# Performance work log

Hardware: AMD Instinct MI355X
Metric: run time of the kernel (lower is better)

Reference implementation:

```python
import jax, jax.numpy as jnp
import numpy as np

B, S, T1, V = 32, 60, 60, 50000   # batch, post len, response len (decoder runs T1-1 steps), vocab
E, A, H, ATT, DI = 300, 300, 512, 512, 512  # word emb, affect emb, rnn hidden, attention size, decoder input


def setup_inputs() -> dict:
    key = jax.random.key(0)
    ks = jax.random.split(key, 20)
    p = lambda i, shape: jax.random.normal(ks[i], shape, jnp.float32) * 0.02
    z = lambda n: jnp.zeros((n,), jnp.float32)
    return {
        'posts': jax.random.randint(ks[0], (B, S), 0, V),
        'responses': jax.random.randint(ks[1], (B, T1), 0, V),
        'len_posts': jnp.full((B,), S, jnp.int32),
        'emb': p(2, (V, E)), 'affect_emb': p(3, (V, A)),
        'enc_Wi': p(4, (3 * H, E)), 'enc_Wh': p(5, (3 * H, H)), 'enc_bi': z(3 * H), 'enc_bh': z(3 * H),
        'aff_Wi': p(6, (3 * H, A)), 'aff_Wh': p(7, (3 * H, H)), 'aff_bi': z(3 * H), 'aff_bh': z(3 * H),
        'Wp': p(8, (H, 2 * H)), 'bp': z(H),
        'Wl': p(9, (DI, E + H + ATT)), 'bl': z(DI),
        'dec_Wi': p(10, (3 * H, DI)), 'dec_Wh': p(11, (3 * H, H)), 'dec_bi': z(3 * H), 'dec_bh': z(3 * H),
        'Wa': p(12, (H, H)), 'Wc': p(13, (ATT, H)), 'bc': z(ATT),
        'Wv': p(14, (V, H + ATT)), 'bv': z(V),
    }


def _gru_cell(x, h, Wi, Wh, bi, bh):
    gi = x @ Wi.T + bi
    gh = h @ Wh.T + bh
    ir, iz, inn = jnp.split(gi, 3, -1)
    hr, hz, hn = jnp.split(gh, 3, -1)
    r = jax.nn.sigmoid(ir + hr)
    zg = jax.nn.sigmoid(iz + hz)
    n = jnp.tanh(inn + r * hn)
    return (1.0 - zg) * n + zg * h


def _gru_seq(xs, h0, Wi, Wh, bi, bh):
    # xs: [S, B, in] -> (outputs [S,B,H], h_last [B,H])
    def step(h, x):
        h2 = _gru_cell(x, h, Wi, Wh, bi, bh)
        return h2, h2
    hT, ys = jax.lax.scan(step, h0, xs)
    return ys, hT


def reference(posts, responses, len_posts, emb, affect_emb,
              enc_Wi, enc_Wh, enc_bi, enc_bh,
              aff_Wi, aff_Wh, aff_bi, aff_bh,
              Wp, bp, Wl, bl,
              dec_Wi, dec_Wh, dec_bi, dec_bh,
              Wa, Wc, bc, Wv, bv):
    embed_posts = emb[posts]            # [B,S,E]
    affect_posts = affect_emb[posts]    # [B,S,A]
    h0 = jnp.zeros((posts.shape[0], H), embed_posts.dtype)

    _, state_encoder = _gru_seq(embed_posts.transpose(1, 0, 2), h0, enc_Wi, enc_Wh, enc_bi, enc_bh)
    out_affect, state_affect = _gru_seq(affect_posts.transpose(1, 0, 2), h0, aff_Wi, aff_Wh, aff_bi, aff_bh)
    context_affect = out_affect[-1]     # [B,H] (all lengths == S)
    K = out_affect.transpose(1, 0, 2)   # [B,S,H] attention keys/values

    # PrepareState: Linear + tanh on concat of both encoder final states
    state0 = jnp.tanh(jnp.concatenate([state_encoder, state_affect], -1) @ Wp.T + bp)

    dec_in = emb[responses[:, :-1]].transpose(1, 0, 2)  # [T,B,E]
    init_attn = jnp.zeros((posts.shape[0], ATT), embed_posts.dtype)

    def dec_step(carry, x_emb):
        h, attn = carry
        x = jnp.concatenate([x_emb, context_affect, attn], -1) @ Wl.T + bl
        h = _gru_cell(x, h, dec_Wi, dec_Wh, dec_bi, dec_bh)
        scores = jnp.einsum('bd,bsd->bs', h @ Wa, K)        # Luong 'general'
        w = jax.nn.softmax(scores, -1)
        ctx = jnp.einsum('bs,bsd->bd', w, K)
        attn = jnp.tanh(ctx @ Wc.T + bc)
        return (h, attn), (jnp.concatenate([h, attn], -1), w)

    _, (outs, weights) = jax.lax.scan(dec_step, (state0, init_attn), dec_in)
    outs = outs.transpose(1, 0, 2)          # [B,T,H+ATT]
    weights = weights.transpose(1, 0, 2)    # [B,T,S]
    output_vocab = jax.nn.softmax(outs @ Wv.T + bv, -1)  # [B,T,V]
    return output_vocab, weights
```

## Files before the change

kernel.cpp:

```cpp
#include <hip/hip_runtime.h>

typedef unsigned int uint32;
typedef unsigned short u16;
typedef unsigned long long u64;
typedef __attribute__((ext_vector_type(8))) short bf8;
typedef __attribute__((ext_vector_type(4))) float f4;
typedef __attribute__((ext_vector_type(4))) uint32 u32x4;

#define DEV static __device__ __forceinline__

DEV f4 MFMA(bf8 a, bf8 b, f4 c) {
  return __builtin_amdgcn_mfma_f32_16x16x32_bf16(a, b, c, 0, 0, 0);
}
DEV u16 f2bf(float f) {
  uint32 u = __float_as_uint(f);
  return (u16)((u + 0x7FFFu + ((u >> 16) & 1u)) >> 16);
}
DEV float bf2f(u16 h) { return __uint_as_float(((uint32)h) << 16); }
DEV float bfLO(uint32 u) { return __uint_as_float(u << 16); }
DEV float bfHI(uint32 u) { return __uint_as_float(u & 0xFFFF0000u); }
DEV float sigmoid_(float x) { return 1.f / (1.f + __expf(-x)); }
DEV float tanh_(float x) {
  float cx = fminf(fmaxf(x, -15.f), 15.f);
  float e = __expf(2.f * cx);
  return (e - 1.f) / (e + 1.f);
}

DEV u64 ldA64(const void* p) {
  return __hip_atomic_load((u64*)p, __ATOMIC_RELAXED, __HIP_MEMORY_SCOPE_AGENT);
}
DEV void stA64(void* p, u64 v) {
  __hip_atomic_store((u64*)p, v, __ATOMIC_RELAXED, __HIP_MEMORY_SCOPE_AGENT);
}
DEV bf8 pk_frag(u64 lo, u64 hi) {
  u32x4 v = {(uint32)lo, (uint32)(lo >> 32), (uint32)hi, (uint32)(hi >> 32)};
  return __builtin_bit_cast(bf8, v);
}

DEV void wait_vm0() { asm volatile("s_waitcnt vmcnt(0)" ::: "memory"); }
DEV void arrive_rlx(int* f) {
  __hip_atomic_fetch_add(f, 1, __ATOMIC_RELAXED, __HIP_MEMORY_SCOPE_AGENT);
}
DEV void wait_rlx(int* f, int tgt) {
  for (int i = 0; i < (1 << 20); ++i) {
    if (__hip_atomic_load(f, __ATOMIC_RELAXED, __HIP_MEMORY_SCOPE_AGENT) >= tgt) return;
    __builtin_amdgcn_s_sleep(1);
  }
}

namespace L {
constexpr size_t o_flags  = 0;
constexpr size_t o_rowsum = 4096;
constexpr size_t o_bcomb  = 11776;
constexpr size_t o_gistat = 17920;
constexpr size_t o_xbuf   = 214528;
constexpr size_t o_henc   = 345600;
constexpr size_t o_haff   = 411136;
constexpr size_t o_cat    = 476672;
constexpr size_t o_Kbuf   = 542208;
constexpr size_t o_KA     = 2508288;
constexpr size_t o_embP   = 4474368;
constexpr size_t o_embA   = 5703168;
constexpr size_t o_embD   = 6931968;
constexpr size_t o_encWi  = 8140288;
constexpr size_t o_affWi  = 9123328;
constexpr size_t o_Whe    = 10106368;
constexpr size_t o_Wha    = 11679232;
constexpr size_t o_decWi  = 13252096;
constexpr size_t o_WlT    = 14824960;
constexpr size_t o_Wa     = 16184832;
constexpr size_t o_Wp     = 16709120;
constexpr size_t o_wq     = 17757696;
constexpr size_t o_Wcomb  = 18281984;
constexpr size_t o_WdE    = 26441216;
constexpr size_t o_WdA    = 27424256;
constexpr size_t o_Wd2    = 28997120;
constexpr size_t o_giE    = 32142848;
constexpr size_t o_giA    = 43939328;
constexpr size_t o_giD    = 55735808;
constexpr size_t o_outsB  = 67335680;
constexpr size_t o_WvB    = 71267840;
constexpr size_t WS_FULL  = 174028288;
constexpr size_t WOFF = 94400000;
}

__global__ __launch_bounds__(256) void kp_gather(
    const int* __restrict__ posts, const int* __restrict__ resp,
    const float* __restrict__ emb, const float* __restrict__ aemb, char* ws)
{
  using namespace L;
  const int gid = blockIdx.x * 256 + threadIdx.x;
  const int r = gid / 320, e = gid - r * 320;
  u16* embP = (u16*)(ws + o_embP);
  u16* embA = (u16*)(ws + o_embA);
  u16* embD = (u16*)(ws + o_embD);
  if (r < 1920) {
    const int b = r & 31, s = r >> 5;
    const int tok = posts[b * 60 + s];
    embP[r * 320 + e] = f2bf(e < 300 ? emb[(size_t)tok * 300 + e] : 0.f);
    embA[r * 320 + e] = f2bf(e < 300 ? aemb[(size_t)tok * 300 + e] : 0.f);
  } else if (r < 3808) {
    const int r2 = r - 1920;
    const int b = r2 & 31, t = r2 >> 5;
    const int tok = resp[b * 60 + t];
    embD[r2 * 320 + e] = f2bf(e < 300 ? emb[(size_t)tok * 300 + e] : 0.f);
  }
}

__global__ __launch_bounds__(256) void kp_wconv(
    const float* __restrict__ encWi, const float* __restrict__ affWi,
    const float* __restrict__ encWh, const float* __restrict__ affWh,
    const float* __restrict__ dWi, const float* __restrict__ Wl,
    const float* __restrict__ Wa, const float* __restrict__ Wp,
    const float* __restrict__ Wc, char* ws)
{
  using namespace L;
  long gid = (long)blockIdx.x * 256 + threadIdx.x;
  if (gid < 983040) {
    const int g = gid >= 491520;
    const long u = gid - (g ? 491520 : 0);
    const int n = (int)(u / 320), e = (int)(u - (long)n * 320);
    const float* src = g ? affWi : encWi;
    u16* dst = (u16*)(ws + (g ? o_affWi : o_encWi));
    dst[u] = f2bf(e < 300 ? src[(size_t)n * 300 + e] : 0.f);
    return;
  }
  gid -= 983040;
  if (gid < 2359296) {
    const int g = (int)(gid / 786432);
    const long u = gid - (long)g * 786432;
    const float* src = g == 0 ? encWh : (g == 1 ? affWh : dWi);
    u16* dst = (u16*)(ws + (g == 0 ? o_Whe : (g == 1 ? o_Wha : o_decWi)));
    dst[u] = f2bf(src[u]);
    return;
  }
  gid -= 2359296;
  if (gid < 679936) {
    const int j = (int)(gid >> 9), k = (int)(gid & 511);
    ((u16*)(ws + o_WlT))[gid] = f2bf(j < 1324 ? Wl[(size_t)k * 1324 + j] : 0.f);
    return;
  }
  gid -= 679936;
  if (gid < 262144) { ((u16*)(ws + o_Wa))[gid] = f2bf(Wa[gid]); return; }
  gid -= 262144;
  if (gid < 524288) { ((u16*)(ws + o_Wp))[gid] = f2bf(Wp[gid]); return; }
  gid -= 524288;
  if (gid < 131072) {
    const int q = (int)(gid & 3), j = (int)((gid >> 2) & 511), g4 = (int)(gid >> 11);
    const int d0 = g4 * 8 + q * 2;
    const uint32 lo = f2bf(Wc[(size_t)j * 512 + d0]);
    const uint32 hi = f2bf(Wc[(size_t)j * 512 + d0 + 1]);
    ((uint32*)(ws + o_wq))[gid] = lo | (hi << 16);
    return;
  }
  gid -= 131072;
  if (gid < 2944) {
    if (gid < 1024) ((uint32*)(ws + o_flags))[gid] = 0;
    else ((uint32*)(ws + o_rowsum))[gid - 1024] = 0;
    return;
  }
  gid -= 2944;
  if (gid < 49152) {
    if (gid < 16384) ((uint32*)(ws + o_outsB + (size_t)1888 * 1024 * 2))[gid] = 0;
    else if (gid < 32768) ((uint32*)(ws + o_henc))[gid - 16384] = 0;
    else ((uint32*)(ws + o_haff))[gid - 32768] = 0;
  }
}

__global__ __launch_bounds__(256) void kp_bcomb(
    const float* __restrict__ dWi, const float* __restrict__ bl,
    const float* __restrict__ dbi, char* ws)
{
  const int i = blockIdx.x * 256 + threadIdx.x;
  if (i >= 1536) return;
  float a = dbi[i];
  for (int k = 0; k < 512; ++k) a += dWi[(size_t)i * 512 + k] * bl[k];
  ((float*)(ws + L::o_bcomb))[i] = a;
}

__global__ __launch_bounds__(256) void kp_wv(const float* __restrict__ Wv, char* ws)
{
  const long gid = (long)blockIdx.x * 256 + threadIdx.x;
  const int r = (int)(gid >> 8), q = (int)(gid & 255);
  u16* WvB = (u16*)(ws + L::o_WvB);
  uint2 o;
  if (r < 50000) {
    const float4 f = *(const float4*)(Wv + (size_t)r * 1024 + q * 4);
    o.x = (uint32)f2bf(f.x) | ((uint32)f2bf(f.y) << 16);
    o.y = (uint32)f2bf(f.z) | ((uint32)f2bf(f.w) << 16);
  } else { o.x = 0u; o.y = 0u; }
  *(uint2*)(WvB + (size_t)r * 1024 + q * 4) = o;
}

__global__ __launch_bounds__(256) void kp_pack2(
    const float* __restrict__ Wcomb, const float* __restrict__ dWh, char* ws)
{
  using namespace L;
  long gid = (long)blockIdx.x * 256 + threadIdx.x;
  if (gid < 491520) {
    const int n = (int)(gid / 320), e = (int)(gid - (long)n * 320);
    ((u16*)(ws + o_WdE))[gid] = f2bf(e < 300 ? Wcomb[(size_t)n * 1328 + e] : 0.f);
    return;
  }
  gid -= 491520;
  if (gid < 786432) {
    const int n = (int)(gid >> 9), k = (int)(gid & 511);
    ((u16*)(ws + o_WdA))[gid] = f2bf(Wcomb[(size_t)n * 1328 + 300 + k]);
    return;
  }
  gid -= 786432;
  if (gid < 1572864) {
    const int n = (int)(gid >> 10), k = (int)(gid & 1023);
    const float v = (k < 512) ? Wcomb[(size_t)n * 1328 + 812 + k]
                              : dWh[(size_t)n * 512 + (k - 512)];
    ((u16*)(ws + o_Wd2))[gid] = f2bf(v);
  }
}

__global__ __launch_bounds__(256) void k_gemm_nt(
    const u16* __restrict__ A, const u16* __restrict__ Bm,
    float* __restrict__ C, const float* __restrict__ bias,
    const int M, const int N, const int Kp)
{
  const int mt = blockIdx.x, cb = blockIdx.y;
  const int w = threadIdx.x >> 6, lane = threadIdx.x & 63;
  const int l15 = lane & 15, lhi = lane >> 4;
  const u16* arow = A + (size_t)(mt * 16 + l15) * Kp + lhi * 8;
  const int c0 = cb * 256 + w * 64;
  f4 acc[4];
#pragma unroll
  for (int nn = 0; nn < 4; ++nn) acc[nn] = (f4){0.f, 0.f, 0.f, 0.f};
  for (int k = 0; k < Kp; k += 32) {
    const bf8 a = *(const bf8*)(arow + k);
#pragma unroll
    for (int nn = 0; nn < 4; ++nn) {
      const int cs = c0 + nn * 16;
      if (cs < N) {
        const bf8 b = *(const bf8*)(Bm + (size_t)(cs + l15) * Kp + k + lhi * 8);
        acc[nn] = MFMA(a, b, acc[nn]);
      }
    }
  }
#pragma unroll
  for (int nn = 0; nn < 4; ++nn) {
    const int cs = c0 + nn * 16;
    if (cs >= N) continue;
    const int c = cs + l15;
    const float bb = bias ? bias[c] : 0.f;
#pragma unroll
    for (int j = 0; j < 4; ++j) {
      const int r = mt * 16 + lhi * 4 + j;
      C[(size_t)r * N + c] = acc[nn][j] + bb;
    }
  }
}

__global__ __launch_bounds__(256, 1) void k_enc(
    char* __restrict__ ws, const float* __restrict__ enc_bh,
    const float* __restrict__ aff_bh)
{
  using namespace L;
  const int tid = threadIdx.x, blk = blockIdx.x;
  const int wave = tid >> 6, lane = tid & 63;
  const int l15 = lane & 15, lhi = lane >> 4;
  const int g = blk >> 5;
  const bool act = wave < 2;
  int* flags = (int*)(ws + o_flags);
  const u16* Wh = (const u16*)(ws + (g ? o_Wha : o_Whe));
  const float* gi = (const float*)(ws + (g ? o_giA : o_giE));
  const float* bh = g ? aff_bh : enc_bh;
  u16* hbuf = (u16*)(ws + (g ? o_haff : o_henc));
  u16* cat = (u16*)(ws + o_cat);
  u16* Kb = (u16*)(ws + o_Kbuf);

  const int wid = (blk & 31) * 2 + (wave & 1);
  const int btile = wid >> 5, ctile = wid & 31;
  const int bl = btile * 16 + l15;
  const int c0 = ctile * 16 + lhi * 4;
  const u16* wr0 = Wh + (size_t)(ctile * 16 + l15) * 512 + lhi * 8;
  const u16* wr1 = wr0 + (size_t)512 * 512;
  const u16* wr2 = wr1 + (size_t)512 * 512;
  f4 bhr4 = {0.f, 0.f, 0.f, 0.f}, bhz4 = bhr4, bhn4 = bhr4;
  if (act) {
    bhr4 = *(const f4*)(bh + c0);
    bhz4 = *(const f4*)(bh + 512 + c0);
    bhn4 = *(const f4*)(bh + 1024 + c0);
  }
  for (int s = 0; s < 60; ++s) {
    const u16* hin = hbuf + (s & 1) * (32 * 512);
    u16* hout = hbuf + ((s & 1) ^ 1) * (32 * 512);
    if (act) {
      const u16* brow = hin + bl * 512 + lhi * 8;
      u64 flo[16], fhi[16];
#pragma unroll
      for (int kk = 0; kk < 16; ++kk) {
        flo[kk] = ldA64(brow + kk * 32);
        fhi[kk] = ldA64(brow + kk * 32 + 4);
      }
      const u64 hq = ldA64(hin + bl * 512 + c0);
      f4 ar = {0.f, 0.f, 0.f, 0.f}, az = ar, an = ar;
#pragma unroll
      for (int kk = 0; kk < 16; ++kk) {
        const bf8 hf = pk_frag(flo[kk], fhi[kk]);
        ar = MFMA(*(const bf8*)(wr0 + kk * 32), hf, ar);
        az = MFMA(*(const bf8*)(wr1 + kk * 32), hf, az);
        an = MFMA(*(const bf8*)(wr2 + kk * 32), hf, an);
      }
      const float* gr = gi + (size_t)(s * 32 + bl) * 1536;
      const f4 g0 = *(const f4*)(gr + c0);
      const f4 g1 = *(const f4*)(gr + 512 + c0);
      const f4 g2 = *(const f4*)(gr + 1024 + c0);
      u64 pk = 0;
#pragma unroll
      for (int j = 0; j < 4; ++j) {
        const float r = sigmoid_(g0[j] + ar[j] + bhr4[j]);
        const float z = sigmoid_(g1[j] + az[j] + bhz4[j]);
        const float n = tanh_(g2[j] + r * (an[j] + bhn4[j]));
        const float hold = bf2f((u16)(hq >> (16 * j)));
        pk |= (u64)f2bf((1.f - z) * n + z * hold) << (16 * j);
      }
      stA64(hout + bl * 512 + c0, pk);
      if (g) *(u64*)(Kb + (size_t)(s * 32 + bl) * 512 + c0) = pk;
      if (s == 59) *(u64*)(cat + bl * 1024 + g * 512 + c0) = pk;
    }
    wait_vm0();
    __syncthreads();
    if (tid == 0) { arrive_rlx(&flags[g * 64 + s]); wait_rlx(&flags[g * 64 + s], 32); }
    __syncthreads();
  }
}

__global__ __launch_bounds__(256) void k_mid(char* __restrict__ ws,
                                             const float* __restrict__ bp)
{
  using namespace L;
  const int tid = threadIdx.x, blk = blockIdx.x;
  const int wave = tid >> 6, lane = tid & 63;
  const int l15 = lane & 15, lhi = lane >> 4;
  u16* xb = (u16*)(ws + o_xbuf);
  u16* cat = (u16*)(ws + o_cat);
  u16* Kb = (u16*)(ws + o_Kbuf);

  if (blk < 16) {
    const u16* Wp_ = (const u16*)(ws + o_Wp);
    const int wid = blk * 4 + wave;
    const int btile = wid >> 5, ctile = wid & 31;
    const int bl = btile * 16 + l15;
    const int c0 = ctile * 16 + lhi * 4;
    const u16* arow = Wp_ + (size_t)(ctile * 16 + l15) * 1024 + lhi * 8;
    const u16* brow = cat + bl * 1024 + lhi * 8;
    f4 acc = {0.f, 0.f, 0.f, 0.f};
    for (int k = 0; k < 1024; k += 32)
      acc = MFMA(*(const bf8*)(arow + k), *(const bf8*)(brow + k), acc);
    const f4 bp4 = *(const f4*)(bp + c0);
    u64 pk = 0;
#pragma unroll
    for (int j = 0; j < 4; ++j)
      pk |= (u64)f2bf(tanh_(acc[j] + bp4[j])) << (16 * j);
    *(u64*)(xb + bl * 1024 + 512 + c0) = pk;
    *(u64*)(xb + bl * 1024 + c0) = 0;
  } else if (blk < 32) {
    const u16* WdA = (const u16*)(ws + o_WdA);
    const float* bco = (const float*)(ws + o_bcomb);
    float* gst = (float*)(ws + o_gistat);
    const int wid = (blk - 16) * 4 + wave;
    const int btile = wid >> 5, ctb = wid & 31;
    const int bl = btile * 16 + l15;
    const int c0 = ctb * 16 + lhi * 4;
    const u16* brow = cat + bl * 1024 + 512 + lhi * 8;
    const u16* a0p = WdA + (size_t)(ctb * 16 + l15) * 512 + lhi * 8;
    const u16* a1p = a0p + (size_t)512 * 512;
    const u16* a2p = a1p + (size_t)512 * 512;
    f4 a0 = {0.f, 0.f, 0.f, 0.f}, a1 = a0, a2 = a0;
    for (int k = 0; k < 512; k += 32) {
      const bf8 bfr = *(const bf8*)(brow + k);
      a0 = MFMA(*(const bf8*)(a0p + k), bfr, a0);
      a1 = MFMA(*(const bf8*)(a1p + k), bfr, a1);
      a2 = MFMA(*(const bf8*)(a2p + k), bfr, a2);
    }
    const f4 v0 = *(const f4*)(bco + c0);
    const f4 v1 = *(const f4*)(bco + 512 + c0);
    const f4 v2 = *(const f4*)(bco + 1024 + c0);
    *(f4*)(gst + bl * 1536 + c0) = a0 + v0;
    *(f4*)(gst + bl * 1536 + 512 + c0) = a1 + v1;
    *(f4*)(gst + bl * 1536 + 1024 + c0) = a2 + v2;
  } else {
    const u16* Wa_ = (const u16*)(ws + o_Wa);
    u16* KAp = (u16*)(ws + o_KA);
    const int widK = (blk - 32) * 4 + wave;
    for (int task = widK; task < 3840; task += 192) {
      const int mt = task >> 5, ct = task & 31;
      const int m = mt * 16 + l15;
      const int c0 = ct * 16 + lhi * 4;
      const u16* arow = Wa_ + (size_t)(ct * 16 + l15) * 512 + lhi * 8;
      const u16* brow = Kb + (size_t)m * 512 + lhi * 8;
      f4 acc = {0.f, 0.f, 0.f, 0.f};
      for (int k = 0; k < 512; k += 32)
        acc = MFMA(*(const bf8*)(arow + k), *(const bf8*)(brow + k), acc);
      u64 pk = 0;
#pragma unroll
      for (int j = 0; j < 4; ++j) pk |= (u64)f2bf(acc[j]) << (16 * j);
      *(u64*)(KAp + (size_t)m * 512 + c0) = pk;
    }
  }
}

__global__ __launch_bounds__(256, 1) void k_dec(
    char* __restrict__ ws, float* __restrict__ out,
    const float* __restrict__ dec_bh, const float* __restrict__ bc)
{
  using namespace L;
  const int tid = threadIdx.x, blk = blockIdx.x;
  const int wave = tid >> 6, lane = tid & 63;
  const int l15 = lane & 15, lhi = lane >> 4;
  int* flags = (int*)(ws + o_flags);

  __shared__ float hsm[512];
  __shared__ float ctxs[512];
  __shared__ float scb[64];
  __shared__ float wsb[64];
  __shared__ u16 attn_sm[256];

  u16* xb = (u16*)(ws + o_xbuf);
  u16* outs = (u16*)(ws + o_outsB);

  if (blk < 32) {
    const bool act = wave < 2;
    const u16* Wd2 = (const u16*)(ws + o_Wd2);
    const float* gst = (const float*)(ws + o_gistat);
    const float* gD = (const float*)(ws + o_giD);
    const int wid = (blk & 31) * 2 + (wave & 1);
    const int btile = wid >> 5, ctile = wid & 31;
    const int bl = btile * 16 + l15;
    const int c0 = ctile * 16 + lhi * 4;
    const u16* wr = Wd2 + (size_t)(ctile * 16 + l15) * 1024 + lhi * 8;
    const u16* wz = wr + (size_t)512 * 1024;
    const u16* wn = wz + (size_t)512 * 1024;
    f4 bhr4 = {0.f, 0.f, 0.f, 0.f}, bhz4 = bhr4, bhn4 = bhr4;
    f4 s0 = bhr4, s1 = bhr4, s2 = bhr4;
    if (act) {
      bhr4 = *(const f4*)(dec_bh + c0);
      bhz4 = *(const f4*)(dec_bh + 512 + c0);
      bhn4 = *(const f4*)(dec_bh + 1024 + c0);
      s0 = *(const f4*)(gst + bl * 1536 + c0);
      s1 = *(const f4*)(gst + bl * 1536 + 512 + c0);
      s2 = *(const f4*)(gst + bl * 1536 + 1024 + c0);
    }
    for (int t = 0; t < 59; ++t) {
      const u16* xin = xb + (t & 1) * (32 * 1024);
      u16* xout = xb + ((t & 1) ^ 1) * (32 * 1024);
      const u16* brow = xin + bl * 1024 + lhi * 8;
      u64 flo[32], fhi[32];
      u64 hq = 0;
      if (t) {
        __syncthreads();
        if (tid == 0) wait_rlx(&flags[384 + (t - 1) * 4], 32);
        __syncthreads();
      }
      if (act) {
#pragma unroll
        for (int kk = 16; kk < 32; ++kk) {
          flo[kk] = ldA64(brow + kk * 32);
          fhi[kk] = ldA64(brow + kk * 32 + 4);
        }
        hq = ldA64(xin + bl * 1024 + 512 + c0);
      }
      if (t) {
        __syncthreads();
        if (tid == 0) wait_rlx(&flags[640 + (t - 1) * 4], 64);
        __syncthreads();
      }
      if (act) {
#pragma unroll
        for (int kk = 0; kk < 16; ++kk) {
          flo[kk] = ldA64(brow + kk * 32);
          fhi[kk] = ldA64(brow + kk * 32 + 4);
        }
        const float* g2p = gD + (size_t)(t * 32 + bl) * 1536;
        const f4 d0 = *(const f4*)(g2p + c0);
        const f4 d1 = *(const f4*)(g2p + 512 + c0);
        const f4 d2 = *(const f4*)(g2p + 1024 + c0);
        f4 ar = {0.f, 0.f, 0.f, 0.f}, az = ar, anx = ar, anh = ar;
#pragma unroll
        for (int kk = 0; kk < 16; ++kk) {
          const bf8 xf = pk_frag(flo[kk], fhi[kk]);
          ar = MFMA(*(const bf8*)(wr + kk * 32), xf, ar);
          az = MFMA(*(const bf8*)(wz + kk * 32), xf, az);
          anx = MFMA(*(const bf8*)(wn + kk * 32), xf, anx);
        }
#pragma unroll
        for (int kk = 16; kk < 32; ++kk) {
          const bf8 xf = pk_frag(flo[kk], fhi[kk]);
          ar = MFMA(*(const bf8*)(wr + kk * 32), xf, ar);
          az = MFMA(*(const bf8*)(wz + kk * 32), xf, az);
          anh = MFMA(*(const bf8*)(wn + kk * 32), xf, anh);
        }
        u64 pk = 0;
#pragma unroll
        for (int j = 0; j < 4; ++j) {
          const float r = sigmoid_(s0[j] + d0[j] + ar[j] + bhr4[j]);
          const float z = sigmoid_(s1[j] + d1[j] + az[j] + bhz4[j]);
          const float n = tanh_(s2[j] + d2[j] + anx[j] + r * (anh[j] + bhn4[j]));
          const float hold = bf2f((u16)(hq >> (16 * j)));
          pk |= (u64)f2bf((1.f - z) * n + z * hold) << (16 * j);
        }
        stA64(xout + bl * 1024 + 512 + c0, pk);
        *(u64*)(outs + (size_t)(bl * 59 + t) * 1024 + c0) = pk;
      }
      wait_vm0();
      __syncthreads();
      if (tid == 0) arrive_rlx(&flags[384 + t * 4]);
    }
  } else {
    const int idx = blk - 32;
    const int b = idx >> 1, half = idx & 1;
    const u16* KAp = (const u16*)(ws + o_KA);
    const u16* Kb = (const u16*)(ws + o_Kbuf);
    const uint4* wq = (const uint4*)(ws + o_wq);
    for (int t = 0; t < 59; ++t) {
      if (tid == 0) wait_rlx(&flags[384 + t * 4], 32);
      __syncthreads();
      const u16* xcur = xb + ((t & 1) ^ 1) * (32 * 1024);
      if (tid < 128) {
        const u64 hv = ldA64(xcur + b * 1024 + 512 + tid * 4);
        const uint32 w0 = (uint32)hv, w1 = (uint32)(hv >> 32);
        hsm[tid * 4 + 0] = bfLO(w0);
        hsm[tid * 4 + 1] = bfHI(w0);
        hsm[tid * 4 + 2] = bfLO(w1);
        hsm[tid * 4 + 3] = bfHI(w1);
      }
      __syncthreads();
      if (tid < 240) {
        const int s = tid >> 2, q = tid & 3;
        const u16* kr = KAp + (size_t)(s * 32 + b) * 512 + q * 128;
        const float* hq = &hsm[q * 128];
        float acc = 0.f;
#pragma unroll 4
        for (int i = 0; i < 128; i += 4) {
          const uint2 k4 = *(const uint2*)(kr + i);
          const float4 h4 = *(const float4*)(hq + i);
          acc += h4.x * bfLO(k4.x) + h4.y * bfHI(k4.x)
               + h4.z * bfLO(k4.y) + h4.w * bfHI(k4.y);
        }
        acc += __shfl_xor(acc, 1);
        acc += __shfl_xor(acc, 2);
        if ((tid & 3) == 0) scb[s] = acc;
      }
      __syncthreads();
      if (tid < 64) {
        const float v = (tid < 60) ? scb[tid] : -1e30f;
        float m = v;
#pragma unroll
        for (int d = 1; d < 64; d <<= 1) m = fmaxf(m, __shfl_xor(m, d));
        const float e = (tid < 60) ? __expf(v - m) : 0.f;
        float sm = e;
#pragma unroll
        for (int d = 1; d < 64; d <<= 1) sm += __shfl_xor(sm, d);
        const float w = e / sm;
        if (tid < 60) {
          wsb[tid] = w;
          if (half == 0) out[WOFF + (size_t)(b * 59 + t) * 60 + tid] = w;
        }
      }
      __syncthreads();
      float c0 = 0.f, c1 = 0.f;
      for (int s = 0; s < 60; ++s) {
        const float w = wsb[s];
        const u16* krow = Kb + (size_t)(s * 32 + b) * 512;
        c0 += w * bf2f(krow[tid]);
        c1 += w * bf2f(krow[tid + 256]);
      }
      ctxs[tid] = c0;
      ctxs[tid + 256] = c1;
      __syncthreads();
      const int jj = half * 256 + tid;
      float fa = bc[jj];
#pragma unroll 2
      for (int g4 = 0; g4 < 64; ++g4) {
        const uint4 wv4 = wq[g4 * 512 + jj];
        const float4 ca = *(const float4*)&ctxs[g4 * 8];
        const float4 cb2 = *(const float4*)&ctxs[g4 * 8 + 4];
        fa += ca.x * bfLO(wv4.x) + ca.y * bfHI(wv4.x);
        fa += ca.z * bfLO(wv4.y) + ca.w * bfHI(wv4.y);
        fa += cb2.x * bfLO(wv4.z) + cb2.y * bfHI(wv4.z);
        fa += cb2.z * bfLO(wv4.w) + cb2.w * bfHI(wv4.w);
      }
      attn_sm[tid] = f2bf(tanh_(fa));
      __syncthreads();
      if (tid < 64) {
        u16* xout = xb + ((t & 1) ^ 1) * (32 * 1024);
        const u64 pk = (u64)attn_sm[tid * 4] | ((u64)attn_sm[tid * 4 + 1] << 16)
                     | ((u64)attn_sm[tid * 4 + 2] << 32) | ((u64)attn_sm[tid * 4 + 3] << 48);
        const int cc = half * 256 + tid * 4;
        stA64(xout + b * 1024 + cc, pk);
        *(u64*)(outs + (size_t)(b * 59 + t) * 1024 + 512 + cc) = pk;
      }
      wait_vm0();
      __syncthreads();
      if (tid == 0) arrive_rlx(&flags[640 + t * 4]);
    }
  }
}

__global__ __launch_bounds__(512, 2) void k_vocab2(
    const u16* __restrict__ A, const u16* __restrict__ Bm,
    const float* __restrict__ bvv, float* __restrict__ out,
    float* __restrict__ rowsum)
{
  __shared__ u16 As[2][128][40];
  __shared__ u16 Bs[2][256][40];
  const int tid = threadIdx.x;
  const int bid = blockIdx.x;
  const int xcd = bid & 7, sub = bid >> 3;
  const int wgid = (xcd < 4 ? xcd * 368 : 4 * 368 + (xcd - 4) * 367) + sub;
  const int mtile = wgid % 15, ntile = wgid / 15;
  const int rbase = mtile * 128, cbase = ntile * 256;

  const int wave = tid >> 6, lane = tid & 63;
  const int l15 = lane & 15, lhi = lane >> 4;
  const int m0 = (wave >> 2) * 64, n0 = (wave & 3) * 64;

  const int sar = tid >> 2, sak = (tid & 3) * 8;
  const u16* gA = A + (size_t)(rbase + sar) * 1024 + sak;
  const u16* gB0 = Bm + (size_t)(cbase + sar) * 1024 + sak;
  const u16* gB1 = Bm + (size_t)(cbase + 128 + sar) * 1024 + sak;

  f4 acc[4][4];
#pragma unroll
  for (int mi = 0; mi < 4; ++mi)
#pragma unroll
    for (int ni = 0; ni < 4; ++ni) acc[mi][ni] = (f4){0.f, 0.f, 0.f, 0.f};

  uint4 ra, rb0, rb1;
  ra = *(const uint4*)(gA);
  rb0 = *(const uint4*)(gB0);
  rb1 = *(const uint4*)(gB1);
  *(uint4*)&As[0][sar][sak] = ra;
  *(uint4*)&Bs[0][sar][sak] = rb0;
  *(uint4*)&Bs[0][128 + sar][sak] = rb1;
  __syncthreads();

  int cur = 0;
#pragma unroll 1
  for (int t = 0; t < 32; ++t) {
    if (t < 31) {
      const int k0 = (t + 1) * 32;
      ra = *(const uint4*)(gA + k0);
      rb0 = *(const uint4*)(gB0 + k0);
      rb1 = *(const uint4*)(gB1 + k0);
    }
    bf8 af[4], bfr[4];
#pragma unroll
    for (int mi = 0; mi < 4; ++mi)
      af[mi] = *(const bf8*)&As[cur][m0 + mi * 16 + l15][lhi * 8];
#pragma unroll
    for (int ni = 0; ni < 4; ++ni)
      bfr[ni] = *(const bf8*)&Bs[cur][n0 + ni * 16 + l15][lhi * 8];
#pragma unroll
    for (int mi = 0; mi < 4; ++mi)
#pragma unroll
      for (int ni = 0; ni < 4; ++ni)
        acc[mi][ni] = MFMA(af[mi], bfr[ni], acc[mi][ni]);
    if (t < 31) {
      __syncthreads();
      *(uint4*)&As[cur ^ 1][sar][sak] = ra;
      *(uint4*)&Bs[cur ^ 1][sar][sak] = rb0;
      *(uint4*)&Bs[cur ^ 1][128 + sar][sak] = rb1;
      __syncthreads();
      cur ^= 1;
    }
  }

#pragma unroll
  for (int mi = 0; mi < 4; ++mi) {
    float rs[4] = {0.f, 0.f, 0.f, 0.f};
#pragma unroll
    for (int ni = 0; ni < 4; ++ni) {
      const int c = cbase + n0 + ni * 16 + l15;
      if (c < 50000) {
        const float bb = bvv[c];
#pragma unroll
        for (int j = 0; j < 4; ++j) {
          const int r = rbase + m0 + mi * 16 + lhi * 4 + j;
          if (r < 1888) {
            const float e = __expf(acc[mi][ni][j] + bb);
            out[(size_t)r * 50000 + c] = e;
            rs[j] += e;
          }
        }
      }
    }
#pragma unroll
    for (int j = 0; j < 4; ++j) {
#pragma unroll
      for (int d = 1; d < 16; d <<= 1) rs[j] += __shfl_xor(rs[j], d);
    }
    if (l15 == 0) {
#pragma unroll
      for (int j = 0; j < 4; ++j) {
        const int r = rbase + m0 + mi * 16 + lhi * 4 + j;
        if (r < 1888) atomicAdd(&rowsum[r], rs[j]);
      }
    }
  }
}

__global__ __launch_bounds__(512) void k_vocab0(
    const u16* __restrict__ A, const float* __restrict__ WvF,
    const float* __restrict__ bv, float* __restrict__ out,
    float* __restrict__ rowsum)
{
  const int bid = blockIdx.x;
  const int x = bid & 7, jj = bid >> 3;
  const int mtile = jj % 15, nseq = jj / 15;
  const int ntile = nseq * 8 + x;
  if (ntile >= 196) return;
  const int w = threadIdx.x >> 6, lane = threadIdx.x & 63;
  const int l15 = lane & 15, lhi = lane >> 4;
  const int rbase = mtile * 128 + w * 16;
  const u16* arow = A + (size_t)(rbase + l15) * 1024 + lhi * 8;
  const int cbase = ntile * 256;
  f4 acc[16];
#pragma unroll
  for (int nn = 0; nn < 16; ++nn) acc[nn] = (f4){0.f, 0.f, 0.f, 0.f};
  for (int k = 0; k < 1024; k += 32) {
    const bf8 a = *(const bf8*)(arow + k);
#pragma unroll
    for (int nn = 0; nn < 16; ++nn) {
      const int cs = cbase + nn * 16;
      bf8 bfr = {0, 0, 0, 0, 0, 0, 0, 0};
      if (cs < 50000) {
        const float* p = WvF + (size_t)(cs + l15) * 1024 + k + lhi * 8;
        const float4 f0 = *(const float4*)p;
        const float4 f1 = *(const float4*)(p + 4);
        bfr[0] = (short)(__float_as_uint(f0.x) >> 16);
        bfr[1] = (short)(__float_as_uint(f0.y) >> 16);
        bfr[2] = (short)(__float_as_uint(f0.z) >> 16);
        bfr[3] = (short)(__float_as_uint(f0.w) >> 16);
        bfr[4] = (short)(__float_as_uint(f1.x) >> 16);
        bfr[5] = (short)(__float_as_uint(f1.y) >> 16);
        bfr[6] = (short)(__float_as_uint(f1.z) >> 16);
        bfr[7] = (short)(__float_as_uint(f1.w) >> 16);
      }
      acc[nn] = MFMA(a, bfr, acc[nn]);
    }
  }
  float rsv[4] = {0.f, 0.f, 0.f, 0.f};
#pragma unroll
  for (int nn = 0; nn < 16; ++nn) {
    const int cs = cbase + nn * 16;
    if (cs >= 50000) continue;
    const int c = cs + l15;
    const float bb = bv[c];
#pragma unroll
    for (int j = 0; j < 4; ++j) {
      const int r = rbase + lhi * 4 + j;
      if (r < 1888) {
        const float e = __expf(acc[nn][j] + bb);
        out[(size_t)r * 50000 + c] = e;
        rsv[j] += e;
      }
    }
  }
#pragma unroll
  for (int j = 0; j < 4; ++j) {
#pragma unroll
    for (int d = 1; d < 16; d <<= 1) rsv[j] += __shfl_xor(rsv[j], d);
  }
  if (l15 == 0) {
#pragma unroll
    for (int j = 0; j < 4; ++j) {
      const int r = rbase + lhi * 4 + j;
      if (r < 1888) atomicAdd(&rowsum[r], rsv[j]);
    }
  }
}

__global__ void k_invrow(float* rs)
{
  const int i = blockIdx.x * 256 + threadIdx.x;
  if (i < 1920) {
    const float s = rs[i];
    rs[i] = (s > 0.f) ? 1.f / s : 0.f;
  }
}

__global__ __launch_bounds__(256) void k_scale(float* __restrict__ out,
                                               const float* __restrict__ inv)
{
  const int bid = blockIdx.x;
  const int r = bid / 49, ch = bid - r * 49;
  const int c = ch * 1024 + threadIdx.x * 4;
  if (c < 50000) {
    const float s = inv[r];
    float4* p = (float4*)(out + (size_t)r * 50000 + c);
    float4 v = *p;
    v.x *= s; v.y *= s; v.z *= s; v.w *= s;
    *p = v;
  }
}

extern "C" void kernel_launch(void* const* d_in, const int* in_sizes, int n_in,
                              void* d_out, int out_size, void* d_ws, size_t ws_size,
                              hipStream_t stream) {
  const int* posts = (const int*)d_in[0];
  const int* resp = (const int*)d_in[1];
  const float* emb = (const float*)d_in[3];
  const float* aemb = (const float*)d_in[4];
  const float* encWi = (const float*)d_in[5];
  const float* encWh = (const float*)d_in[6];
  const float* enc_bi = (const float*)d_in[7];
  const float* enc_bh = (const float*)d_in[8];
  const float* affWi = (const float*)d_in[9];
  const float* affWh = (const float*)d_in[10];
  const float* aff_bi = (const float*)d_in[11];
  const float* aff_bh = (const float*)d_in[12];
  const float* Wp = (const float*)d_in[13];
  const float* bp = (const float*)d_in[14];
  const float* Wl = (const float*)d_in[15];
  const float* bl = (const float*)d_in[16];
  const float* dWi = (const float*)d_in[17];
  const float* dWh = (const float*)d_in[18];
  const float* dbi = (const float*)d_in[19];
  const float* dbh = (const float*)d_in[20];
  const float* Wa = (const float*)d_in[21];
  const float* Wc = (const float*)d_in[22];
  const float* bc = (const float*)d_in[23];
  const float* Wv = (const float*)d_in[24];
  const float* bv = (const float*)d_in[25];
  char* ws = (char*)d_ws;
  float* out = (float*)d_out;
  const bool useWvB = ws_size >= L::WS_FULL;

  kp_gather<<<4760, 256, 0, stream>>>(posts, resp, emb, aemb, ws);
  kp_wconv<<<19500, 256, 0, stream>>>(encWi, affWi, encWh, affWh, dWi, Wl, Wa, Wp, Wc, ws);
  kp_bcomb<<<6, 256, 0, stream>>>(dWi, bl, dbi, ws);
  if (useWvB) kp_wv<<<50176, 256, 0, stream>>>(Wv, ws);

  k_gemm_nt<<<dim3(96, 6), 256, 0, stream>>>(
      (const u16*)(ws + L::o_decWi), (const u16*)(ws + L::o_WlT),
      (float*)(ws + L::o_Wcomb), nullptr, 1536, 1328, 512);
  kp_pack2<<<11136, 256, 0, stream>>>((const float*)(ws + L::o_Wcomb), dWh, ws);

  k_gemm_nt<<<dim3(120, 6), 256, 0, stream>>>(
      (const u16*)(ws + L::o_embP), (const u16*)(ws + L::o_encWi),
      (float*)(ws + L::o_giE), enc_bi, 1920, 1536, 320);
  k_gemm_nt<<<dim3(120, 6), 256, 0, stream>>>(
      (const u16*)(ws + L::o_embA), (const u16*)(ws + L::o_affWi),
      (float*)(ws + L::o_giA), aff_bi, 1920, 1536, 320);
  k_gemm_nt<<<dim3(118, 6), 256, 0, stream>>>(
      (const u16*)(ws + L::o_embD), (const u16*)(ws + L::o_WdE),
      (float*)(ws + L::o_giD), nullptr, 1888, 1536, 320);

  k_enc<<<64, 256, 0, stream>>>(ws, enc_bh, aff_bh);
  k_mid<<<80, 256, 0, stream>>>(ws, bp);
  k_dec<<<96, 256, 0, stream>>>(ws, out, dbh, bc);

  if (useWvB)
    k_vocab2<<<2940, 512, 0, stream>>>(
        (const u16*)(ws + L::o_outsB), (const u16*)(ws + L::o_WvB),
        bv, out, (float*)(ws + L::o_rowsum));
  else
    k_vocab0<<<2944, 512, 0, stream>>>(
        (const u16*)(ws + L::o_outsB), Wv, bv, out, (float*)(ws + L::o_rowsum));

  k_invrow<<<8, 256, 0, stream>>>((float*)(ws + L::o_rowsum));
  k_scale<<<92512, 256, 0, stream>>>(out, (const float*)(ws + L::o_rowsum));
}
```

Baseline: 2.692 ms.

## Replace atomic counter barriers with per-block progress slots and split dependent MFMA

Grid-wide barriers built on fetch_add counters are replaced by per-block progress slots: each block stores its step number and one wave polls all slots with a wave-wide __all check. The aim is to cut atomic contention and the serial single-thread polling on the encoder and decoder recurrences. The decoder GRU now issues the hidden-state half of its MFMAs before waiting on the attention blocks, so that work overlaps the wait, and the attention dot products use several independent accumulators to shorten dependency chains. This relies on monotonic slot values and on the flag region being zeroed and laid out to match the new offsets.

```diff
diff --git a/kernel.cpp b/kernel.cpp
--- a/kernel.cpp
+++ b/kernel.cpp
@@ -32,18 +32,23 @@
 DEV void stA64(void* p, u64 v) {
   __hip_atomic_store((u64*)p, v, __ATOMIC_RELAXED, __HIP_MEMORY_SCOPE_AGENT);
 }
+DEV void stA32(int* p, int v) {
+  __hip_atomic_store(p, v, __ATOMIC_RELAXED, __HIP_MEMORY_SCOPE_AGENT);
+}
 DEV bf8 pk_frag(u64 lo, u64 hi) {
   u32x4 v = {(uint32)lo, (uint32)(lo >> 32), (uint32)hi, (uint32)(hi >> 32)};
   return __builtin_bit_cast(bf8, v);
 }
 
 DEV void wait_vm0() { asm volatile("s_waitcnt vmcnt(0)" ::: "memory"); }
-DEV void arrive_rlx(int* f) {
-  __hip_atomic_fetch_add(f, 1, __ATOMIC_RELAXED, __HIP_MEMORY_SCOPE_AGENT);
-}
-DEV void wait_rlx(int* f, int tgt) {
+DEV void wait_slots(const int* slots, int n, int tgt) {
+  const int lane = threadIdx.x & 63;
   for (int i = 0; i < (1 << 20); ++i) {
-    if (__hip_atomic_load(f, __ATOMIC_RELAXED, __HIP_MEMORY_SCOPE_AGENT) >= tgt) return;
+    int v = 0x7fffffff;
+    if (lane < n)
+      v = __hip_atomic_load((int*)(slots + lane), __ATOMIC_RELAXED,
+                            __HIP_MEMORY_SCOPE_AGENT);
+    if (__all(v >= tgt)) return;
     __builtin_amdgcn_s_sleep(1);
   }
 }
@@ -266,6 +271,7 @@
   const int g = blk >> 5;
   const bool act = wave < 2;
   int* flags = (int*)(ws + o_flags);
+  int* slotE = flags + 128 + g * 64;
   const u16* Wh = (const u16*)(ws + (g ? o_Wha : o_Whe));
   const float* gi = (const float*)(ws + (g ? o_giA : o_giE));
   const float* bh = g ? aff_bh : enc_bh;
@@ -325,7 +331,8 @@
     }
     wait_vm0();
     __syncthreads();
-    if (tid == 0) { arrive_rlx(&flags[g * 64 + s]); wait_rlx(&flags[g * 64 + s], 32); }
+    if (tid == 0) stA32(&slotE[blk & 31], s + 1);
+    if (wave == 2) wait_slots(slotE, 32, s + 1);
     __syncthreads();
   }
 }
@@ -414,6 +421,8 @@
   const int wave = tid >> 6, lane = tid & 63;
   const int l15 = lane & 15, lhi = lane >> 4;
   int* flags = (int*)(ws + o_flags);
+  int* slotA = flags;
+  int* slotB = flags + 64;
 
   __shared__ float hsm[512];
   __shared__ float ctxs[512];
@@ -450,50 +459,50 @@
       const u16* xin = xb + (t & 1) * (32 * 1024);
       u16* xout = xb + ((t & 1) ^ 1) * (32 * 1024);
       const u16* brow = xin + bl * 1024 + lhi * 8;
-      u64 flo[32], fhi[32];
+      f4 ar = {0.f, 0.f, 0.f, 0.f}, az = ar, anx = ar, anh = ar;
       u64 hq = 0;
+      f4 d0 = ar, d1 = ar, d2 = ar;
       if (t) {
+        if (wave == 2) wait_slots(slotA, 32, t);
         __syncthreads();
-        if (tid == 0) wait_rlx(&flags[384 + (t - 1) * 4], 32);
-        __syncthreads();
       }
       if (act) {
-#pragma unroll
-        for (int kk = 16; kk < 32; ++kk) {
-          flo[kk] = ldA64(brow + kk * 32);
-          fhi[kk] = ldA64(brow + kk * 32 + 4);
+        u64 flo[16], fhi[16];
+#pragma unroll
+        for (int kk = 0; kk < 16; ++kk) {
+          flo[kk] = ldA64(brow + (16 + kk) * 32);
+          fhi[kk] = ldA64(brow + (16 + kk) * 32 + 4);
         }
         hq = ldA64(xin + bl * 1024 + 512 + c0);
-      }
-      if (t) {
-        __syncthreads();
-        if (tid == 0) wait_rlx(&flags[640 + (t - 1) * 4], 64);
-        __syncthreads();
-      }
-      if (act) {
-#pragma unroll
-        for (int kk = 0; kk < 16; ++kk) {
-          flo[kk] = ldA64(brow + kk * 32);
-          fhi[kk] = ldA64(brow + kk * 32 + 4);
-        }
         const float* g2p = gD + (size_t)(t * 32 + bl) * 1536;
-        const f4 d0 = *(const f4*)(g2p + c0);
-        const f4 d1 = *(const f4*)(g2p + 512 + c0);
-        const f4 d2 = *(const f4*)(g2p + 1024 + c0);
-        f4 ar = {0.f, 0.f, 0.f, 0.f}, az = ar, anx = ar, anh = ar;
+        d0 = *(const f4*)(g2p + c0);
+        d1 = *(const f4*)(g2p + 512 + c0);
+        d2 = *(const f4*)(g2p + 1024 + c0);
 #pragma unroll
         for (int kk = 0; kk < 16; ++kk) {
           const bf8 xf = pk_frag(flo[kk], fhi[kk]);
+          ar = MFMA(*(const bf8*)(wr + (16 + kk) * 32), xf, ar);
+          az = MFMA(*(const bf8*)(wz + (16 + kk) * 32), xf, az);
+          anh = MFMA(*(const bf8*)(wn + (16 + kk) * 32), xf, anh);
+        }
+      }
+      if (t) {
+        if (wave == 2) wait_slots(slotB, 64, t);
+        __syncthreads();
+      }
+      if (act) {
+        u64 glo[16], ghi[16];
+#pragma unroll
+        for (int kk = 0; kk < 16; ++kk) {
+          glo[kk] = ldA64(brow + kk * 32);
+          ghi[kk] = ldA64(brow + kk * 32 + 4);
+        }
+#pragma unroll
+        for (int kk = 0; kk < 16; ++kk) {
+          const bf8 xf = pk_frag(glo[kk], ghi[kk]);
           ar = MFMA(*(const bf8*)(wr + kk * 32), xf, ar);
           az = MFMA(*(const bf8*)(wz + kk * 32), xf, az);
           anx = MFMA(*(const bf8*)(wn + kk * 32), xf, anx);
-        }
-#pragma unroll
-        for (int kk = 16; kk < 32; ++kk) {
-          const bf8 xf = pk_frag(flo[kk], fhi[kk]);
-          ar = MFMA(*(const bf8*)(wr + kk * 32), xf, ar);
-          az = MFMA(*(const bf8*)(wz + kk * 32), xf, az);
-          anh = MFMA(*(const bf8*)(wn + kk * 32), xf, anh);
         }
         u64 pk = 0;
 #pragma unroll
@@ -509,7 +518,7 @@
       }
       wait_vm0();
       __syncthreads();
-      if (tid == 0) arrive_rlx(&flags[384 + t * 4]);
+      if (tid == 0) stA32(&slotA[blk], t + 1);
     }
   } else {
     const int idx = blk - 32;
@@ -518,7 +527,7 @@
     const u16* Kb = (const u16*)(ws + o_Kbuf);
     const uint4* wq = (const uint4*)(ws + o_wq);
     for (int t = 0; t < 59; ++t) {
-      if (tid == 0) wait_rlx(&flags[384 + t * 4], 32);
+      if (wave == 0) wait_slots(slotA, 32, t + 1);
       __syncthreads();
       const u16* xcur = xb + ((t & 1) ^ 1) * (32 * 1024);
       if (tid < 128) {
@@ -534,14 +543,19 @@
         const int s = tid >> 2, q = tid & 3;
         const u16* kr = KAp + (size_t)(s * 32 + b) * 512 + q * 128;
         const float* hq = &hsm[q * 128];
-        float acc = 0.f;
+        float acc0 = 0.f, acc1 = 0.f;
 #pragma unroll 4
-        for (int i = 0; i < 128; i += 4) {
+        for (int i = 0; i < 128; i += 8) {
           const uint2 k4 = *(const uint2*)(kr + i);
+          const uint2 k5 = *(const uint2*)(kr + i + 4);
           const float4 h4 = *(const float4*)(hq + i);
-          acc += h4.x * bfLO(k4.x) + h4.y * bfHI(k4.x)
-               + h4.z * bfLO(k4.y) + h4.w * bfHI(k4.y);
+          const float4 h5 = *(const float4*)(hq + i + 4);
+          acc0 += h4.x * bfLO(k4.x) + h4.y * bfHI(k4.x)
+                + h4.z * bfLO(k4.y) + h4.w * bfHI(k4.y);
+          acc1 += h5.x * bfLO(k5.x) + h5.y * bfHI(k5.x)
+                + h5.z * bfLO(k5.y) + h5.w * bfHI(k5.y);
         }
+        float acc = acc0 + acc1;
         acc += __shfl_xor(acc, 1);
         acc += __shfl_xor(acc, 2);
         if ((tid & 3) == 0) scb[s] = acc;
@@ -563,28 +577,37 @@
         }
       }
       __syncthreads();
-      float c0 = 0.f, c1 = 0.f;
-      for (int s = 0; s < 60; ++s) {
-        const float w = wsb[s];
-        const u16* krow = Kb + (size_t)(s * 32 + b) * 512;
-        c0 += w * bf2f(krow[tid]);
-        c1 += w * bf2f(krow[tid + 256]);
-      }
-      ctxs[tid] = c0;
-      ctxs[tid + 256] = c1;
+      {
+        float c0a = 0.f, c0b = 0.f, c1a = 0.f, c1b = 0.f;
+#pragma unroll 2
+        for (int s = 0; s < 60; s += 2) {
+          const float w0 = wsb[s], w1 = wsb[s + 1];
+          const u16* kr0 = Kb + (size_t)(s * 32 + b) * 512;
+          const u16* kr1 = Kb + (size_t)((s + 1) * 32 + b) * 512;
+          c0a += w0 * bf2f(kr0[tid]);
+          c1a += w0 * bf2f(kr0[tid + 256]);
+          c0b += w1 * bf2f(kr1[tid]);
+          c1b += w1 * bf2f(kr1[tid + 256]);
+        }
+        ctxs[tid] = c0a + c0b;
+        ctxs[tid + 256] = c1a + c1b;
+      }
       __syncthreads();
       const int jj = half * 256 + tid;
-      float fa = bc[jj];
-#pragma unroll 2
+      float faa[4] = {0.f, 0.f, 0.f, 0.f};
+      float fbb[4] = {0.f, 0.f, 0.f, 0.f};
+#pragma unroll 4
       for (int g4 = 0; g4 < 64; ++g4) {
         const uint4 wv4 = wq[g4 * 512 + jj];
         const float4 ca = *(const float4*)&ctxs[g4 * 8];
         const float4 cb2 = *(const float4*)&ctxs[g4 * 8 + 4];
-        fa += ca.x * bfLO(wv4.x) + ca.y * bfHI(wv4.x);
-        fa += ca.z * bfLO(wv4.y) + ca.w * bfHI(wv4.y);
-        fa += cb2.x * bfLO(wv4.z) + cb2.y * bfHI(wv4.z);
-        fa += cb2.z * bfLO(wv4.w) + cb2.w * bfHI(wv4.w);
-      }
+        faa[g4 & 3] += ca.x * bfLO(wv4.x) + ca.y * bfHI(wv4.x)
+                     + ca.z * bfLO(wv4.y) + ca.w * bfHI(wv4.y);
+        fbb[g4 & 3] += cb2.x * bfLO(wv4.z) + cb2.y * bfHI(wv4.z)
+                     + cb2.z * bfLO(wv4.w) + cb2.w * bfHI(wv4.w);
+      }
+      const float fa = bc[jj] + faa[0] + faa[1] + faa[2] + faa[3]
+                     + fbb[0] + fbb[1] + fbb[2] + fbb[3];
       attn_sm[tid] = f2bf(tanh_(fa));
       __syncthreads();
       if (tid < 64) {
@@ -597,7 +620,7 @@
       }
       wait_vm0();
       __syncthreads();
-      if (tid == 0) arrive_rlx(&flags[640 + t * 4]);
+      if (tid == 0) stA32(&slotB[idx], t + 1);
     }
   }
 }
```

Measured after the change: 2.574 ms. -4.4%, faster.
